# Optimization experiments

Measured on AMD Instinct MI355X. Metric: run time of the kernel, lower is better.

Reference implementation:

```python
import jax, jax.numpy as jnp
import numpy as np


def _sepconv1x1(x, dw, pw, b):
    # SeparableConv2D with kernel=1: depthwise 1x1 = per-channel scale, then pointwise matmul
    return jnp.einsum('nhwc,cd->nhwd', x * dw, pw) + b


def setup_inputs() -> dict:
    key = jax.random.key(0)
    ks = jax.random.split(key, 12)
    N, H, W, C_in, C_red = 4, 64, 64, 256, 64
    s = 0.05  # small init so softmax logits are well-conditioned
    return {
        'feature_maps': jax.random.normal(ks[0], (N, H, W, C_in), jnp.float32),
        'global_channel_output': jax.random.normal(ks[1], (N, H, W, C_in), jnp.float32),
        'dw_q': jax.random.normal(ks[2], (C_in,), jnp.float32) * s,
        'pw_q': jax.random.normal(ks[3], (C_in, C_red), jnp.float32) * s,
        'b_q': jnp.zeros((C_red,), jnp.float32),
        'dw_k': jax.random.normal(ks[4], (C_in,), jnp.float32) * s,
        'pw_k': jax.random.normal(ks[5], (C_in, C_red), jnp.float32) * s,
        'b_k': jnp.zeros((C_red,), jnp.float32),
        'dw_v': jax.random.normal(ks[6], (C_in,), jnp.float32) * s,
        'pw_v': jax.random.normal(ks[7], (C_in, C_red), jnp.float32) * s,
        'b_v': jnp.zeros((C_red,), jnp.float32),
        'dw_a': jax.random.normal(ks[8], (C_red,), jnp.float32) * s,
        'pw_a': jax.random.normal(ks[9], (C_red, C_in), jnp.float32) * s,
        'b_a': jnp.zeros((C_in,), jnp.float32),
    }


def reference(feature_maps, global_channel_output,
              dw_q, pw_q, b_q, dw_k, pw_k, b_k, dw_v, pw_v, b_v,
              dw_a, pw_a, b_a):
    N, H, W, _ = feature_maps.shape
    q = _sepconv1x1(feature_maps, dw_q, pw_q, b_q)  # [N,H,W,Cr]
    k = _sepconv1x1(feature_maps, dw_k, pw_k, b_k)
    v = _sepconv1x1(feature_maps, dw_v, pw_v, b_v)
    Cr = q.shape[-1]
    q = q.reshape(N, H * W, Cr)
    k = k.reshape(N, H * W, Cr)
    v = v.reshape(N, H * W, Cr)
    # tf.matmul(key, query, transpose_b=True): scores[i,j] = key_i . query_j
    scores = jnp.einsum('nic,njc->nij', k, q)  # [N,HW,HW]
    scores = jax.nn.softmax(scores, axis=-1)
    # tf.matmul(value, scores, transpose_a=True) -> [N,Cr,HW]
    att = jnp.einsum('nic,nij->ncj', v, scores)
    # faithful raw reshape (as in the original TF code) from [N,Cr,HW] to [N,H,W,Cr]
    att = att.reshape(N, H, W, Cr)
    att = _sepconv1x1(att, dw_a, pw_a, b_a)  # [N,H,W,C_in]
    return global_channel_output * att + global_channel_output
```

## Files before the change

### kernel.cpp

```cpp
#include <hip/hip_runtime.h>
#include <hip/hip_bf16.h>

typedef __attribute__((ext_vector_type(8))) __bf16 bf16x8;
typedef __attribute__((ext_vector_type(4))) float floatx4;
typedef __attribute__((ext_vector_type(2))) unsigned short us2;
typedef __attribute__((ext_vector_type(4))) unsigned short us4;
typedef __attribute__((ext_vector_type(8))) unsigned short us8;
typedef __attribute__((ext_vector_type(4))) short s16x4;
typedef __attribute__((ext_vector_type(2))) unsigned int uint2v;

#define MFMA16(A, B, C) __builtin_amdgcn_mfma_f32_16x16x32_bf16((A), (B), (C), 0, 0, 0)
#define MFMA1K(A, B, C) __builtin_amdgcn_mfma_f32_16x16x16bf16_1k((A), (B), (C), 0, 0, 0)

static __device__ __forceinline__ unsigned short f2bfbits(float f) {
    __hip_bfloat16 h = __float2bfloat16(f);
    union { __hip_bfloat16 h; unsigned short u; } cv;
    cv.h = h;
    return cv.u;
}
static __device__ __forceinline__ unsigned int rne32(float f) {
    unsigned int u = __builtin_bit_cast(unsigned int, f);
    return u + 0x7fffu + ((u >> 16) & 1u);
}
static __device__ __forceinline__ unsigned short rne16(float f) {
    return (unsigned short)(rne32(f) >> 16);
}
static __device__ __forceinline__ s16x4 pack4(float e0, float e1, float e2, float e3) {
    unsigned int pa = __builtin_amdgcn_perm(rne32(e1), rne32(e0), 0x07060302u);
    unsigned int pb = __builtin_amdgcn_perm(rne32(e3), rne32(e2), 0x07060302u);
    uint2v u = {pa, pb};
    return __builtin_bit_cast(s16x4, u);
}
static __device__ __forceinline__ bf16x8 load_bf8(const __hip_bfloat16* p) {
    return *reinterpret_cast<const bf16x8*>(p);
}
static __device__ __forceinline__ bf16x8 cvt8(floatx4 a, floatx4 b) {
    us8 u;
#pragma unroll
    for (int i = 0; i < 4; i++) { u[i] = rne16(a[i]); u[4 + i] = rne16(b[i]); }
    return __builtin_bit_cast(bf16x8, u);
}
static __device__ __forceinline__ float bf2f(unsigned short u) {
    unsigned int w = ((unsigned int)u) << 16;
    return __builtin_bit_cast(float, w);
}


__global__ __launch_bounds__(256) void prep_w(
    const float* __restrict__ dwq, const float* __restrict__ pwq,
    const float* __restrict__ dwk, const float* __restrict__ pwk,
    const float* __restrict__ dwv, const float* __restrict__ pwv,
    __hip_bfloat16* __restrict__ wT)
{
    int idx = blockIdx.x * 256 + threadIdx.x;
    int p = idx >> 14;
    int r = idx & 16383;
    int d = r >> 8, c = r & 255;
    const float* dw = (p == 0) ? dwq : ((p == 1) ? dwk : dwv);
    const float* pw = (p == 0) ? pwq : ((p == 1) ? pwk : pwv);
    wT[idx] = __float2bfloat16(dw[c] * pw[c * 64 + d]);
}

__global__ __launch_bounds__(256) void proj_qkv(
    const float* __restrict__ x,
    const __hip_bfloat16* __restrict__ wT,
    const float* __restrict__ bqp, const float* __restrict__ bkp,
    const float* __restrict__ bvp,
    __hip_bfloat16* __restrict__ qf, __hip_bfloat16* __restrict__ kf,
    __hip_bfloat16* __restrict__ vf)
{
    int wid = blockIdx.x * 4 + (threadIdx.x >> 6);
    int lane = threadIdx.x & 63;
    int l15 = lane & 15, quad = lane >> 4;
    int strip = wid << 4;

    floatx4 acc[3][4];
#pragma unroll
    for (int p = 0; p < 3; p++)
#pragma unroll
        for (int t = 0; t < 4; t++) acc[p][t] = (floatx4){0.f, 0.f, 0.f, 0.f};

    const float* xrow = x + (strip + l15) * 256 + quad * 8;
#pragma unroll
    for (int ks = 0; ks < 8; ks++) {
        floatx4 xa = *reinterpret_cast<const floatx4*>(xrow + ks * 32);
        floatx4 xb = *reinterpret_cast<const floatx4*>(xrow + ks * 32 + 4);
        bf16x8 a = cvt8(xa, xb);
#pragma unroll
        for (int p = 0; p < 3; p++)
#pragma unroll
            for (int t = 0; t < 4; t++) {
                bf16x8 b = load_bf8(wT + p * 16384 + (t * 16 + l15) * 256 + ks * 32 + quad * 8);
                acc[p][t] = MFMA16(a, b, acc[p][t]);
            }
    }
#pragma unroll
    for (int p = 0; p < 2; p++) {
        __hip_bfloat16* dst = (p == 0) ? qf : kf;
        const float* bias = (p == 0) ? bqp : bkp;
#pragma unroll
        for (int t = 0; t < 4; t++) {
            float bsv = bias[t * 16 + l15];
            int off0 = wid * 1024 + (t >> 1) * 512 +
                       (((((t & 1) << 1) | (l15 >> 3)) * 16 + quad * 4) * 8) + (l15 & 7);
#pragma unroll
            for (int r = 0; r < 4; r++)
                dst[off0 + r * 8] = __float2bfloat16(acc[p][t][r] + bsv);
        }
    }
#pragma unroll
    for (int t = 0; t < 4; t++) {
        float bsv = bvp[t * 16 + l15];
        us4 pk;
#pragma unroll
        for (int r = 0; r < 4; r++) pk[r] = f2bfbits(acc[2][t][r] + bsv);
        *reinterpret_cast<us4*>(vf + (wid * 4 + t) * 256 + lane * 4) = pk;
    }
}

__global__ __launch_bounds__(512) void pass1_rl(
    const __hip_bfloat16* __restrict__ qf, const __hip_bfloat16* __restrict__ kf,
    const __hip_bfloat16* __restrict__ vf, __hip_bfloat16* __restrict__ vfs)
{
    int itg = blockIdx.x;
    int n = itg >> 8;
    int jw = threadIdx.x >> 6;
    int lane = threadIdx.x & 63;
    int l15 = lane & 15, quad = lane >> 4;

    const __hip_bfloat16* kp = kf + itg * 1024;
    bf16x8 a0 = load_bf8(kp + lane * 8);
    bf16x8 a1 = load_bf8(kp + 512 + lane * 8);

    float ls0 = 0.f, ls1 = 0.f, ls2 = 0.f, ls3 = 0.f;
    const __hip_bfloat16* qp0 = qf + (n * 256 + jw * 32) * 1024 + lane * 8;
    for (int it = 0; it < 16; it++, qp0 += 2048) {
        bf16x8 b0 = load_bf8(qp0);
        bf16x8 b1 = load_bf8(qp0 + 512);
        bf16x8 b2 = load_bf8(qp0 + 1024);
        bf16x8 b3 = load_bf8(qp0 + 1536);
        floatx4 s0 = (floatx4){0.f, 0.f, 0.f, 0.f};
        floatx4 s1 = (floatx4){0.f, 0.f, 0.f, 0.f};
        s0 = MFMA16(a0, b0, s0);
        s0 = MFMA16(a1, b1, s0);
        s1 = MFMA16(a0, b2, s1);
        s1 = MFMA16(a1, b3, s1);
        ls0 += __expf(s0[0]) + __expf(s1[0]);
        ls1 += __expf(s0[1]) + __expf(s1[1]);
        ls2 += __expf(s0[2]) + __expf(s1[2]);
        ls3 += __expf(s0[3]) + __expf(s1[3]);
    }
#pragma unroll
    for (int m = 1; m < 16; m <<= 1) {
        ls0 += __shfl_xor(ls0, m, 64);
        ls1 += __shfl_xor(ls1, m, 64);
        ls2 += __shfl_xor(ls2, m, 64);
        ls3 += __shfl_xor(ls3, m, 64);
    }
    __shared__ float red[8][16];
    __shared__ float rls[16];
    if (l15 == 0) {
        red[jw][quad * 4 + 0] = ls0;
        red[jw][quad * 4 + 1] = ls1;
        red[jw][quad * 4 + 2] = ls2;
        red[jw][quad * 4 + 3] = ls3;
    }
    __syncthreads();
    if (threadIdx.x < 16) {
        float tot = 0.f;
#pragma unroll
        for (int w = 0; w < 8; w++) tot += red[w][threadIdx.x];
        rls[threadIdx.x] = 1.0f / tot;
    }
    __syncthreads();
    int m0 = threadIdx.x * 2;
    us2 vv = *reinterpret_cast<const us2*>(reinterpret_cast<const unsigned short*>(vf) + itg * 1024 + m0);
    int r0 = ((m0 >> 6) & 3) * 4 + (m0 & 3);
    us2 ov;
    ov[0] = rne16(bf2f(vv[0]) * rls[r0]);
    ov[1] = rne16(bf2f(vv[1]) * rls[r0 + 1]);
    *reinterpret_cast<us2*>(reinterpret_cast<unsigned short*>(vfs) + itg * 1024 + m0) = ov;
}

__global__ __launch_bounds__(256) void pass2_att(
    const __hip_bfloat16* __restrict__ qf, const __hip_bfloat16* __restrict__ kf,
    const __hip_bfloat16* __restrict__ vfs,
    unsigned short* __restrict__ attp)
{
    int b = blockIdx.x;
    int ih = b & 7;
    int g = b >> 3;
    int n = g >> 6;
    int jg = g & 63;
    int w = threadIdx.x >> 6;
    int jt = jg * 4 + w;
    int lane = threadIdx.x & 63;
    int l15 = lane & 15, quad = lane >> 4;

    const __hip_bfloat16* qp = qf + (n * 256 + jt) * 1024;
    bf16x8 bq0 = load_bf8(qp + lane * 8);
    bf16x8 bq1 = load_bf8(qp + 512 + lane * 8);

    floatx4 acc[4];
#pragma unroll
    for (int t = 0; t < 4; t++) acc[t] = (floatx4){0.f, 0.f, 0.f, 0.f};

    int it0 = n * 256 + ih * 32;
    const __hip_bfloat16* kp = kf + it0 * 1024 + lane * 8;
    const __hip_bfloat16* vp = vfs + it0 * 1024;
    for (int it = 0; it < 32; it++, kp += 1024, vp += 1024) {
        bf16x8 a0 = load_bf8(kp);
        bf16x8 a1 = load_bf8(kp + 512);
        floatx4 s = (floatx4){0.f, 0.f, 0.f, 0.f};
        s = MFMA16(a0, bq0, s);
        s = MFMA16(a1, bq1, s);
        s16x4 p = pack4(__expf(s[0]), __expf(s[1]), __expf(s[2]), __expf(s[3]));
#pragma unroll
        for (int t = 0; t < 4; t++) {
            s16x4 bv = *reinterpret_cast<const s16x4*>(vp + t * 256 + lane * 4);
            acc[t] = MFMA1K(p, bv, acc[t]);
        }
    }
    unsigned short* op0 = attp + ih * 1048576;
#pragma unroll
    for (int t = 0; t < 4; t++) {
        s16x4 pk = pack4(acc[t][0], acc[t][1], acc[t][2], acc[t][3]);
        unsigned short* op = op0 + (n * 64 + t * 16 + l15) * 4096 + jt * 16 + quad * 4;
        *reinterpret_cast<s16x4*>(op) = pk;
    }
}

__global__ __launch_bounds__(256) void final_out(
    const unsigned short* __restrict__ attp, const float* __restrict__ gco,
    const float* __restrict__ dwa, const float* __restrict__ pwa,
    const float* __restrict__ ba, float* __restrict__ out)
{
    int b = blockIdx.x;
    int n = b >> 9;
    int hh = (b >> 3) & 63;
    int w0 = (b & 7) << 3;
    __shared__ float g[512];
    int tid = threadIdx.x;
    const unsigned short* ap = attp + (n * 64 + hh) * 4096 + w0 * 64;
    for (int jj = tid; jj < 512; jj += 256) {
        float v = 0.f;
#pragma unroll
        for (int ph = 0; ph < 8; ph++) v += bf2f(ap[ph * 1048576 + jj]);
        g[jj] = v * dwa[jj & 63];
    }
    __syncthreads();
    float acc[8];
#pragma unroll
    for (int w = 0; w < 8; w++) acc[w] = 0.f;
    for (int cc = 0; cc < 64; cc++) {
        float p = pwa[cc * 256 + tid];
#pragma unroll
        for (int w = 0; w < 8; w++) acc[w] += g[w * 64 + cc] * p;
    }
    float bb = ba[tid];
#pragma unroll
    for (int w = 0; w < 8; w++) {
        int pos = (n * 64 + hh) * 64 + w0 + w;
        float gv = gco[pos * 256 + tid];
        out[pos * 256 + tid] = gv * (acc[w] + bb) + gv;
    }
}

extern "C" void kernel_launch(void* const* d_in, const int* in_sizes, int n_in,
                              void* d_out, int out_size, void* d_ws, size_t ws_size,
                              hipStream_t stream) {
    const float* x   = (const float*)d_in[0];
    const float* gco = (const float*)d_in[1];
    const float* dwq = (const float*)d_in[2];
    const float* pwq = (const float*)d_in[3];
    const float* bq  = (const float*)d_in[4];
    const float* dwk = (const float*)d_in[5];
    const float* pwk = (const float*)d_in[6];
    const float* bk  = (const float*)d_in[7];
    const float* dwv = (const float*)d_in[8];
    const float* pwv = (const float*)d_in[9];
    const float* bv  = (const float*)d_in[10];
    const float* dwa = (const float*)d_in[11];
    const float* pwa = (const float*)d_in[12];
    const float* ba  = (const float*)d_in[13];
    float* out = (float*)d_out;

    char* ws = (char*)d_ws;
    __hip_bfloat16* wT  = (__hip_bfloat16*)ws;
    __hip_bfloat16* qf  = (__hip_bfloat16*)(ws + 98304);
    __hip_bfloat16* kf  = (__hip_bfloat16*)(ws + 2195456);
    __hip_bfloat16* vf  = (__hip_bfloat16*)(ws + 4292608);
    __hip_bfloat16* vfs = (__hip_bfloat16*)(ws + 6389760);
    unsigned short* attp = (unsigned short*)(ws + 8486912);

    prep_w<<<192, 256, 0, stream>>>(dwq, pwq, dwk, pwk, dwv, pwv, wT);
    proj_qkv<<<256, 256, 0, stream>>>(x, wT, bq, bk, bv, qf, kf, vf);
    pass1_rl<<<1024, 512, 0, stream>>>(qf, kf, vf, vfs);
    pass2_att<<<2048, 256, 0, stream>>>(qf, kf, vfs, attp);
    final_out<<<2048, 256, 0, stream>>>(attp, gco, dwa, pwa, ba, out);
}
```

Before: 202.2 us.

## Rebalance tiling: split projection per output, double tiles in attention passes

The projection kernel now gives each wave one of q/k/v instead of all three. That triples the grid and cuts accumulator registers. pass1 processes two key tiles per block so each loaded query tile is reused, and pass2 processes two query tiles per wave so each loaded K/V tile feeds twice the MFMA work. The intent is to reduce global load traffic per FLOP in the attention passes and to improve occupancy or parallelism in the projection. The trade-off is higher register use and half as many blocks in the attention kernels.

```diff
diff --git a/kernel.cpp b/kernel.cpp
--- a/kernel.cpp
+++ b/kernel.cpp
@@ -3,7 +3,6 @@
 
 typedef __attribute__((ext_vector_type(8))) __bf16 bf16x8;
 typedef __attribute__((ext_vector_type(4))) float floatx4;
-typedef __attribute__((ext_vector_type(2))) unsigned short us2;
 typedef __attribute__((ext_vector_type(4))) unsigned short us4;
 typedef __attribute__((ext_vector_type(8))) unsigned short us8;
 typedef __attribute__((ext_vector_type(4))) short s16x4;
@@ -69,33 +68,31 @@
     __hip_bfloat16* __restrict__ qf, __hip_bfloat16* __restrict__ kf,
     __hip_bfloat16* __restrict__ vf)
 {
-    int wid = blockIdx.x * 4 + (threadIdx.x >> 6);
+    int wg = blockIdx.x * 4 + (threadIdx.x >> 6);
+    int p = wg >> 10;
+    int wid = wg & 1023;
     int lane = threadIdx.x & 63;
     int l15 = lane & 15, quad = lane >> 4;
     int strip = wid << 4;
 
-    floatx4 acc[3][4];
-#pragma unroll
-    for (int p = 0; p < 3; p++)
-#pragma unroll
-        for (int t = 0; t < 4; t++) acc[p][t] = (floatx4){0.f, 0.f, 0.f, 0.f};
+    floatx4 acc[4];
+#pragma unroll
+    for (int t = 0; t < 4; t++) acc[t] = (floatx4){0.f, 0.f, 0.f, 0.f};
 
     const float* xrow = x + (strip + l15) * 256 + quad * 8;
+    const __hip_bfloat16* wp = wT + p * 16384;
 #pragma unroll
     for (int ks = 0; ks < 8; ks++) {
         floatx4 xa = *reinterpret_cast<const floatx4*>(xrow + ks * 32);
         floatx4 xb = *reinterpret_cast<const floatx4*>(xrow + ks * 32 + 4);
         bf16x8 a = cvt8(xa, xb);
 #pragma unroll
-        for (int p = 0; p < 3; p++)
-#pragma unroll
-            for (int t = 0; t < 4; t++) {
-                bf16x8 b = load_bf8(wT + p * 16384 + (t * 16 + l15) * 256 + ks * 32 + quad * 8);
-                acc[p][t] = MFMA16(a, b, acc[p][t]);
-            }
-    }
-#pragma unroll
-    for (int p = 0; p < 2; p++) {
+        for (int t = 0; t < 4; t++) {
+            bf16x8 b = load_bf8(wp + (t * 16 + l15) * 256 + ks * 32 + quad * 8);
+            acc[t] = MFMA16(a, b, acc[t]);
+        }
+    }
+    if (p < 2) {
         __hip_bfloat16* dst = (p == 0) ? qf : kf;
         const float* bias = (p == 0) ? bqp : bkp;
 #pragma unroll
@@ -105,16 +102,17 @@
                        (((((t & 1) << 1) | (l15 >> 3)) * 16 + quad * 4) * 8) + (l15 & 7);
 #pragma unroll
             for (int r = 0; r < 4; r++)
-                dst[off0 + r * 8] = __float2bfloat16(acc[p][t][r] + bsv);
-        }
-    }
-#pragma unroll
-    for (int t = 0; t < 4; t++) {
-        float bsv = bvp[t * 16 + l15];
-        us4 pk;
-#pragma unroll
-        for (int r = 0; r < 4; r++) pk[r] = f2bfbits(acc[2][t][r] + bsv);
-        *reinterpret_cast<us4*>(vf + (wid * 4 + t) * 256 + lane * 4) = pk;
+                dst[off0 + r * 8] = __float2bfloat16(acc[t][r] + bsv);
+        }
+    } else {
+#pragma unroll
+        for (int t = 0; t < 4; t++) {
+            float bsv = bvp[t * 16 + l15];
+            us4 pk;
+#pragma unroll
+            for (int r = 0; r < 4; r++) pk[r] = f2bfbits(acc[t][r] + bsv);
+            *reinterpret_cast<us4*>(vf + (wid * 4 + t) * 256 + lane * 4) = pk;
+        }
     }
 }
 
@@ -122,64 +120,72 @@
     const __hip_bfloat16* __restrict__ qf, const __hip_bfloat16* __restrict__ kf,
     const __hip_bfloat16* __restrict__ vf, __hip_bfloat16* __restrict__ vfs)
 {
-    int itg = blockIdx.x;
-    int n = itg >> 8;
+    int itg0 = blockIdx.x * 2;
+    int n = itg0 >> 8;
     int jw = threadIdx.x >> 6;
     int lane = threadIdx.x & 63;
     int l15 = lane & 15, quad = lane >> 4;
 
-    const __hip_bfloat16* kp = kf + itg * 1024;
-    bf16x8 a0 = load_bf8(kp + lane * 8);
-    bf16x8 a1 = load_bf8(kp + 512 + lane * 8);
-
-    float ls0 = 0.f, ls1 = 0.f, ls2 = 0.f, ls3 = 0.f;
+    const __hip_bfloat16* kp = kf + itg0 * 1024 + lane * 8;
+    bf16x8 a0 = load_bf8(kp);
+    bf16x8 a1 = load_bf8(kp + 512);
+    bf16x8 a2 = load_bf8(kp + 1024);
+    bf16x8 a3 = load_bf8(kp + 1536);
+
+    floatx4 lsA = (floatx4){0.f, 0.f, 0.f, 0.f};
+    floatx4 lsB = (floatx4){0.f, 0.f, 0.f, 0.f};
     const __hip_bfloat16* qp0 = qf + (n * 256 + jw * 32) * 1024 + lane * 8;
     for (int it = 0; it < 16; it++, qp0 += 2048) {
         bf16x8 b0 = load_bf8(qp0);
         bf16x8 b1 = load_bf8(qp0 + 512);
         bf16x8 b2 = load_bf8(qp0 + 1024);
         bf16x8 b3 = load_bf8(qp0 + 1536);
-        floatx4 s0 = (floatx4){0.f, 0.f, 0.f, 0.f};
-        floatx4 s1 = (floatx4){0.f, 0.f, 0.f, 0.f};
-        s0 = MFMA16(a0, b0, s0);
-        s0 = MFMA16(a1, b1, s0);
-        s1 = MFMA16(a0, b2, s1);
-        s1 = MFMA16(a1, b3, s1);
-        ls0 += __expf(s0[0]) + __expf(s1[0]);
-        ls1 += __expf(s0[1]) + __expf(s1[1]);
-        ls2 += __expf(s0[2]) + __expf(s1[2]);
-        ls3 += __expf(s0[3]) + __expf(s1[3]);
+        floatx4 z = (floatx4){0.f, 0.f, 0.f, 0.f};
+        floatx4 sA0 = MFMA16(a1, b1, MFMA16(a0, b0, z));
+        floatx4 sA1 = MFMA16(a1, b3, MFMA16(a0, b2, z));
+        floatx4 sB0 = MFMA16(a3, b1, MFMA16(a2, b0, z));
+        floatx4 sB1 = MFMA16(a3, b3, MFMA16(a2, b2, z));
+#pragma unroll
+        for (int r = 0; r < 4; r++) {
+            lsA[r] += __expf(sA0[r]) + __expf(sA1[r]);
+            lsB[r] += __expf(sB0[r]) + __expf(sB1[r]);
+        }
     }
 #pragma unroll
     for (int m = 1; m < 16; m <<= 1) {
-        ls0 += __shfl_xor(ls0, m, 64);
-        ls1 += __shfl_xor(ls1, m, 64);
-        ls2 += __shfl_xor(ls2, m, 64);
-        ls3 += __shfl_xor(ls3, m, 64);
-    }
-    __shared__ float red[8][16];
-    __shared__ float rls[16];
+#pragma unroll
+        for (int r = 0; r < 4; r++) {
+            lsA[r] += __shfl_xor(lsA[r], m, 64);
+            lsB[r] += __shfl_xor(lsB[r], m, 64);
+        }
+    }
+    __shared__ float red[8][32];
+    __shared__ float rls[32];
     if (l15 == 0) {
-        red[jw][quad * 4 + 0] = ls0;
-        red[jw][quad * 4 + 1] = ls1;
-        red[jw][quad * 4 + 2] = ls2;
-        red[jw][quad * 4 + 3] = ls3;
+#pragma unroll
+        for (int r = 0; r < 4; r++) {
+            red[jw][quad * 4 + r] = lsA[r];
+            red[jw][16 + quad * 4 + r] = lsB[r];
+        }
     }
     __syncthreads();
-    if (threadIdx.x < 16) {
+    if (threadIdx.x < 32) {
         float tot = 0.f;
 #pragma unroll
         for (int w = 0; w < 8; w++) tot += red[w][threadIdx.x];
         rls[threadIdx.x] = 1.0f / tot;
     }
     __syncthreads();
-    int m0 = threadIdx.x * 2;
-    us2 vv = *reinterpret_cast<const us2*>(reinterpret_cast<const unsigned short*>(vf) + itg * 1024 + m0);
-    int r0 = ((m0 >> 6) & 3) * 4 + (m0 & 3);
-    us2 ov;
-    ov[0] = rne16(bf2f(vv[0]) * rls[r0]);
-    ov[1] = rne16(bf2f(vv[1]) * rls[r0 + 1]);
-    *reinterpret_cast<us2*>(reinterpret_cast<unsigned short*>(vfs) + itg * 1024 + m0) = ov;
+    int m0 = threadIdx.x * 4;
+    int toff = m0 >> 10;
+    int mm = m0 & 1023;
+    int rb = toff * 16 + ((mm >> 6) & 3) * 4;
+    const unsigned short* vin = reinterpret_cast<const unsigned short*>(vf) + itg0 * 1024 + m0;
+    us4 vv = *reinterpret_cast<const us4*>(vin);
+    us4 ov;
+#pragma unroll
+    for (int r = 0; r < 4; r++) ov[r] = rne16(bf2f(vv[r]) * rls[rb + r]);
+    *reinterpret_cast<us4*>(reinterpret_cast<unsigned short*>(vfs) + itg0 * 1024 + m0) = ov;
 }
 
 __global__ __launch_bounds__(256) void pass2_att(
@@ -190,20 +196,25 @@
     int b = blockIdx.x;
     int ih = b & 7;
     int g = b >> 3;
-    int n = g >> 6;
-    int jg = g & 63;
+    int n = g >> 5;
+    int jg = g & 31;
     int w = threadIdx.x >> 6;
-    int jt = jg * 4 + w;
+    int jt0 = jg * 8 + w * 2;
     int lane = threadIdx.x & 63;
     int l15 = lane & 15, quad = lane >> 4;
 
-    const __hip_bfloat16* qp = qf + (n * 256 + jt) * 1024;
-    bf16x8 bq0 = load_bf8(qp + lane * 8);
-    bf16x8 bq1 = load_bf8(qp + 512 + lane * 8);
-
-    floatx4 acc[4];
-#pragma unroll
-    for (int t = 0; t < 4; t++) acc[t] = (floatx4){0.f, 0.f, 0.f, 0.f};
+    const __hip_bfloat16* qp = qf + (n * 256 + jt0) * 1024 + lane * 8;
+    bf16x8 bq00 = load_bf8(qp);
+    bf16x8 bq01 = load_bf8(qp + 512);
+    bf16x8 bq10 = load_bf8(qp + 1024);
+    bf16x8 bq11 = load_bf8(qp + 1536);
+
+    floatx4 acc0[4], acc1[4];
+#pragma unroll
+    for (int t = 0; t < 4; t++) {
+        acc0[t] = (floatx4){0.f, 0.f, 0.f, 0.f};
+        acc1[t] = (floatx4){0.f, 0.f, 0.f, 0.f};
+    }
 
     int it0 = n * 256 + ih * 32;
     const __hip_bfloat16* kp = kf + it0 * 1024 + lane * 8;
@@ -211,22 +222,30 @@
     for (int it = 0; it < 32; it++, kp += 1024, vp += 1024) {
         bf16x8 a0 = load_bf8(kp);
         bf16x8 a1 = load_bf8(kp + 512);
-        floatx4 s = (floatx4){0.f, 0.f, 0.f, 0.f};
-        s = MFMA16(a0, bq0, s);
-        s = MFMA16(a1, bq1, s);
-        s16x4 p = pack4(__expf(s[0]), __expf(s[1]), __expf(s[2]), __expf(s[3]));
+        floatx4 z = (floatx4){0.f, 0.f, 0.f, 0.f};
+        floatx4 s0a = MFMA16(a0, bq00, z);
+        floatx4 s0b = MFMA16(a1, bq01, z);
+        floatx4 s1a = MFMA16(a0, bq10, z);
+        floatx4 s1b = MFMA16(a1, bq11, z);
+        floatx4 s0 = s0a + s0b;
+        floatx4 s1 = s1a + s1b;
+        s16x4 p0 = pack4(__expf(s0[0]), __expf(s0[1]), __expf(s0[2]), __expf(s0[3]));
+        s16x4 p1 = pack4(__expf(s1[0]), __expf(s1[1]), __expf(s1[2]), __expf(s1[3]));
 #pragma unroll
         for (int t = 0; t < 4; t++) {
             s16x4 bv = *reinterpret_cast<const s16x4*>(vp + t * 256 + lane * 4);
-            acc[t] = MFMA1K(p, bv, acc[t]);
+            acc0[t] = MFMA1K(p0, bv, acc0[t]);
+            acc1[t] = MFMA1K(p1, bv, acc1[t]);
         }
     }
     unsigned short* op0 = attp + ih * 1048576;
 #pragma unroll
     for (int t = 0; t < 4; t++) {
-        s16x4 pk = pack4(acc[t][0], acc[t][1], acc[t][2], acc[t][3]);
-        unsigned short* op = op0 + (n * 64 + t * 16 + l15) * 4096 + jt * 16 + quad * 4;
-        *reinterpret_cast<s16x4*>(op) = pk;
+        s16x4 k0 = pack4(acc0[t][0], acc0[t][1], acc0[t][2], acc0[t][3]);
+        s16x4 k1 = pack4(acc1[t][0], acc1[t][1], acc1[t][2], acc1[t][3]);
+        unsigned short* op = op0 + (n * 64 + t * 16 + l15) * 4096 + jt0 * 16 + quad * 4;
+        *reinterpret_cast<s16x4*>(op) = k0;
+        *reinterpret_cast<s16x4*>(op + 16) = k1;
     }
 }
 
@@ -294,8 +313,8 @@
     unsigned short* attp = (unsigned short*)(ws + 8486912);
 
     prep_w<<<192, 256, 0, stream>>>(dwq, pwq, dwk, pwk, dwv, pwv, wT);
-    proj_qkv<<<256, 256, 0, stream>>>(x, wT, bq, bk, bv, qf, kf, vf);
-    pass1_rl<<<1024, 512, 0, stream>>>(qf, kf, vf, vfs);
-    pass2_att<<<2048, 256, 0, stream>>>(qf, kf, vfs, attp);
+    proj_qkv<<<768, 256, 0, stream>>>(x, wT, bq, bk, bv, qf, kf, vf);
+    pass1_rl<<<512, 512, 0, stream>>>(qf, kf, vf, vfs);
+    pass2_att<<<1024, 256, 0, stream>>>(qf, kf, vfs, attp);
     final_out<<<2048, 256, 0, stream>>>(attp, gco, dwa, pwa, ba, out);
 }
```

After: 182.6 us. 1.11x faster.
